# Performance work log

Hardware: AMD Instinct MI355X
Metric: run time of the kernel (lower is better)

## Reference

```python
import jax, jax.numpy as jnp
import numpy as np

GS = 8      # grid_size
NH = 8      # num_heads
DM = 256    # hidden_dim / d_model
B, W, H = 4, 256, 256


def setup_inputs() -> dict:
    key = jax.random.key(0)
    ks = jax.random.split(key, 5)
    s = 0.02
    return {
        "x": jax.random.normal(ks[0], (B, DM, W, H), dtype=jnp.float32),
        "Wq": jax.random.normal(ks[1], (DM, DM), dtype=jnp.float32) * s,
        "bq": jnp.zeros((DM,), dtype=jnp.float32),
        "Wk": jax.random.normal(ks[2], (DM, DM), dtype=jnp.float32) * s,
        "bk": jnp.zeros((DM,), dtype=jnp.float32),
        "Wv": jax.random.normal(ks[3], (DM, DM), dtype=jnp.float32) * s,
        "bv": jnp.zeros((DM,), dtype=jnp.float32),
        "Wo": jax.random.normal(ks[4], (DM, DM), dtype=jnp.float32) * s,
        "bo": jnp.zeros((DM,), dtype=jnp.float32),
    }


def reference(x, Wq, bq, Wk, bk, Wv, bv, Wo, bo):
    b, d, w, h = x.shape
    gw, gh = w // GS, h // GS
    n = gw * gh               # num grid cells
    L = GS * GS               # tokens per cell
    dh = d // NH

    # query: avg-pool each grid cell -> (b*n, 1, d)
    q = x.reshape(b, d, gw, GS, gh, GS).mean(axis=(3, 5))      # (b, d, gw, gh)
    q = q.reshape(b, d, n).transpose(0, 2, 1).reshape(b * n, 1, d)

    # K/V: per-cell patch tokens, (b*n, L, d); matches torch unfold layout
    kv = x.transpose(0, 2, 3, 1)                                # (b, w, h, d)
    kv = kv.reshape(b, gw, GS, gh, GS, d)
    kv = kv.transpose(0, 1, 3, 2, 4, 5).reshape(b * n, L, d)

    # multi-head cross-attention (standard: q/k/v/out linear + softmax)
    qp = (q @ Wq.T + bq).reshape(b * n, 1, NH, dh).transpose(0, 2, 1, 3)   # (bn, H, 1, dh)
    kp = (kv @ Wk.T + bk).reshape(b * n, L, NH, dh).transpose(0, 2, 1, 3)  # (bn, H, L, dh)
    vp = (kv @ Wv.T + bv).reshape(b * n, L, NH, dh).transpose(0, 2, 1, 3)

    scores = jnp.einsum("bhqd,bhkd->bhqk", qp, kp) / jnp.sqrt(jnp.float32(dh))
    attn = jax.nn.softmax(scores, axis=-1)                      # (bn, H, 1, L)
    ctx = jnp.einsum("bhqk,bhkd->bhqd", attn, vp)               # (bn, H, 1, dh)
    ctx = ctx.transpose(0, 2, 1, 3).reshape(b * n, 1, d)
    attn_out = ctx @ Wo.T + bo                                  # (bn, 1, d)

    out = q + attn_out
    return out.reshape(b, n, d)
```

## Files before the change

kernel.cpp:

```cpp
#include <hip/hip_runtime.h>
#include <hip/hip_bf16.h>


#define NCELL 4096

typedef float f32x4 __attribute__((ext_vector_type(4)));
typedef short s16x8 __attribute__((ext_vector_type(8)));

#define OFF_NT 0u
#define OFF_BE 262144u
#define OFF_Q 262400u
#define OFF_S 1310976u
#define OFF_WQB 5505280u
#define OFF_WKB 5538048u

__device__ __forceinline__ unsigned short bfrnd(float f) {
  unsigned u = __float_as_uint(f);
  u += 0x7fffu + ((u >> 16) & 1u);
  return (unsigned short)(u >> 16);
}
__device__ __forceinline__ float bflo(unsigned u) { return __uint_as_float(u << 16); }
__device__ __forceinline__ float bfhi(unsigned u) { return __uint_as_float(u & 0xffff0000u); }

__global__ __launch_bounds__(256) void k_cvt(const float* __restrict__ Wq, const float* __restrict__ Wk,
                                             unsigned short* __restrict__ WQB, unsigned short* __restrict__ WKB) {
  const int i = blockIdx.x * 256 + threadIdx.x;
  {
    const float4 v = *reinterpret_cast<const float4*>(Wq + i * 4);
    const unsigned lo = (unsigned)bfrnd(v.x) | ((unsigned)bfrnd(v.y) << 16);
    const unsigned hi = (unsigned)bfrnd(v.z) | ((unsigned)bfrnd(v.w) << 16);
    *reinterpret_cast<uint2*>(WQB + i * 4) = make_uint2(lo, hi);
  }
  {
    const float4 v = *reinterpret_cast<const float4*>(Wk + i * 4);
    const unsigned lo = (unsigned)bfrnd(v.x) | ((unsigned)bfrnd(v.y) << 16);
    const unsigned hi = (unsigned)bfrnd(v.z) | ((unsigned)bfrnd(v.w) << 16);
    *reinterpret_cast<uint2*>(WKB + i * 4) = make_uint2(lo, hi);
  }
}

__global__ __launch_bounds__(256) void k_nt(const float* __restrict__ Wv, const float* __restrict__ Wo,
                                            unsigned short* __restrict__ NT) {
  __shared__ float wo_s[32];
  const int n = blockIdx.x >> 3, h = blockIdx.x & 7;
  const int j = threadIdx.x;
  if (threadIdx.x < 32) wo_s[threadIdx.x] = Wo[n * 256 + h * 32 + threadIdx.x];
  __syncthreads();
  float acc = 0.f;
#pragma unroll
  for (int i = 0; i < 32; ++i) acc += Wv[(h * 32 + i) * 256 + j] * wo_s[i];
  NT[(size_t)n * 2048 + h * 256 + j] = bfrnd(acc);
}

__global__ __launch_bounds__(256) void k_beff(const float* __restrict__ bo, const float* __restrict__ bv,
                                              const float* __restrict__ Wo, float* __restrict__ BE) {
  const int w = threadIdx.x >> 6, l = threadIdx.x & 63;
  const int k = blockIdx.x * 4 + w;
  float acc = 0.f;
#pragma unroll
  for (int c = 0; c < 4; ++c) acc += bv[l + 64 * c] * Wo[k * 256 + l + 64 * c];
#pragma unroll
  for (int mk = 32; mk >= 1; mk >>= 1) acc += __shfl_xor(acc, mk);
  if (l == 0) BE[k] = acc + bo[k];
}

__global__ __launch_bounds__(256) void k_cell(
    const float* __restrict__ x,
    const unsigned short* __restrict__ WQB, const float* __restrict__ bq,
    const unsigned short* __restrict__ WKB, const float* __restrict__ bk,
    float* __restrict__ Qg, unsigned short* __restrict__ Sg) {
  __shared__ __align__(16) unsigned short xb[256 * 72];
  __shared__ __align__(16) float q_s[256];
  __shared__ __align__(16) float qp_s[256];
  __shared__ __align__(16) unsigned short r_bf[8 * 264];
  __shared__ __align__(16) float R1[2304];
  __shared__ float off_s[8];

  const int tid = threadIdx.x;
  const int cell = blockIdx.x;
  const int b = cell >> 10, cw = (cell >> 5) & 31, ch = cell & 31;
  const float* xp = x + (size_t)b * 16777216 + (size_t)cw * 2048 + (size_t)ch * 8;

#pragma unroll
  for (int it = 0; it < 16; ++it) {
    const int idx = it * 256 + tid;
    const int d = idx >> 4, i = (idx >> 1) & 7, half = idx & 1;
    const float4 v = *reinterpret_cast<const float4*>(xp + (size_t)d * 65536 + i * 256 + half * 4);
    const int t0 = i * 8 + half * 4;
    const unsigned lo = (unsigned)bfrnd(v.x) | ((unsigned)bfrnd(v.y) << 16);
    const unsigned hi = (unsigned)bfrnd(v.z) | ((unsigned)bfrnd(v.w) << 16);
    *reinterpret_cast<uint2*>(&xb[d * 72 + t0]) = make_uint2(lo, hi);
    float ps = (v.x + v.y) + (v.z + v.w);
    ps += __shfl_xor(ps, 1);
    ps += __shfl_xor(ps, 2);
    ps += __shfl_xor(ps, 4);
    ps += __shfl_xor(ps, 8);
    if ((tid & 15) == 0) {
      const float qv = ps * (1.0f / 64.0f);
      q_s[d] = qv;
      Qg[(size_t)cell * 256 + d] = qv;
    }
  }
  __syncthreads();

  {
    const int io = tid >> 5, jl = tid & 31;
    const float4 qa = *reinterpret_cast<const float4*>(&q_s[jl * 8]);
    const float4 qb = *reinterpret_cast<const float4*>(&q_s[jl * 8 + 4]);
#pragma unroll 4
    for (int r = 0; r < 32; ++r) {
      const int i = r * 8 + io;
      const uint4 wv = *reinterpret_cast<const uint4*>(WQB + i * 256 + jl * 8);
      float acc = bflo(wv.x) * qa.x + bfhi(wv.x) * qa.y + bflo(wv.y) * qa.z + bfhi(wv.y) * qa.w +
                  bflo(wv.z) * qb.x + bfhi(wv.z) * qb.y + bflo(wv.w) * qb.z + bfhi(wv.w) * qb.w;
      acc += __shfl_xor(acc, 16);
      acc += __shfl_xor(acc, 8);
      acc += __shfl_xor(acc, 4);
      acc += __shfl_xor(acc, 2);
      acc += __shfl_xor(acc, 1);
      if (jl == 0) qp_s[i] = (acc + bq[i]) * 0.17677669529663689f;
    }
  }
  __syncthreads();

  {
    const int hw = tid >> 6;
    const int j0 = (tid & 63) * 4;
#pragma unroll
    for (int hh = 0; hh < 2; ++hh) {
      const int h = hw * 2 + hh;
      float a0 = 0.f, a1 = 0.f, a2 = 0.f, a3 = 0.f;
#pragma unroll
      for (int i = 0; i < 32; ++i) {
        const float s = qp_s[h * 32 + i];
        const uint2 wv = *reinterpret_cast<const uint2*>(WKB + (h * 32 + i) * 256 + j0);
        a0 += s * bflo(wv.x);
        a1 += s * bfhi(wv.x);
        a2 += s * bflo(wv.y);
        a3 += s * bfhi(wv.y);
      }
      const unsigned lo = (unsigned)bfrnd(a0) | ((unsigned)bfrnd(a1) << 16);
      const unsigned hi = (unsigned)bfrnd(a2) | ((unsigned)bfrnd(a3) << 16);
      *reinterpret_cast<uint2*>(&r_bf[h * 264 + j0]) = make_uint2(lo, hi);
    }
    if (tid < 8) {
      float o = 0.f;
      for (int i = 0; i < 32; ++i) o += qp_s[tid * 32 + i] * bk[tid * 32 + i];
      off_s[tid] = o;
    }
  }
  __syncthreads();

  {
    const int t = tid & 63, p = tid >> 6;
    float xr[64];
#pragma unroll
    for (int dd = 0; dd < 64; ++dd) {
      const unsigned v = xb[(p * 64 + dd) * 72 + t];
      xr[dd] = __uint_as_float(v << 16);
    }
#pragma unroll
    for (int h = 0; h < 8; ++h) {
      float acc = 0.f;
#pragma unroll
      for (int dc = 0; dc < 8; ++dc) {
        const uint4 rv = *reinterpret_cast<const uint4*>(&r_bf[h * 264 + p * 64 + dc * 8]);
        acc += bflo(rv.x) * xr[dc * 8 + 0] + bfhi(rv.x) * xr[dc * 8 + 1] +
               bflo(rv.y) * xr[dc * 8 + 2] + bfhi(rv.y) * xr[dc * 8 + 3] +
               bflo(rv.z) * xr[dc * 8 + 4] + bfhi(rv.z) * xr[dc * 8 + 5] +
               bflo(rv.w) * xr[dc * 8 + 6] + bfhi(rv.w) * xr[dc * 8 + 7];
      }
      R1[p * 576 + t * 9 + h] = acc;
    }
  }
  __syncthreads();

  {
    const int w = tid >> 6, t = tid & 63;
    float av[2];
#pragma unroll
    for (int hi = 0; hi < 2; ++hi) {
      const int h = w + hi * 4;
      const float v = R1[0 * 576 + t * 9 + h] + R1[1 * 576 + t * 9 + h] +
                      R1[2 * 576 + t * 9 + h] + R1[3 * 576 + t * 9 + h] + off_s[h];
      float m = v;
#pragma unroll
      for (int mk = 32; mk >= 1; mk >>= 1) m = fmaxf(m, __shfl_xor(m, mk));
      const float e = __expf(v - m);
      float s = e;
#pragma unroll
      for (int mk = 32; mk >= 1; mk >>= 1) s += __shfl_xor(s, mk);
      av[hi] = e / s;
    }
    __syncthreads();
    R1[t * 12 + w] = av[0];
    R1[t * 12 + w + 4] = av[1];
  }
  __syncthreads();

  {
    const int d = tid;
    float acc[8] = {0, 0, 0, 0, 0, 0, 0, 0};
#pragma unroll
    for (int tc = 0; tc < 8; ++tc) {
      const uint4 xv = *reinterpret_cast<const uint4*>(&xb[d * 72 + tc * 8]);
      const float xf[8] = {bflo(xv.x), bfhi(xv.x), bflo(xv.y), bfhi(xv.y),
                           bflo(xv.z), bfhi(xv.z), bflo(xv.w), bfhi(xv.w)};
#pragma unroll
      for (int k = 0; k < 8; ++k) {
        const int t = tc * 8 + k;
        const float4 aA = *reinterpret_cast<const float4*>(&R1[t * 12]);
        const float4 aB = *reinterpret_cast<const float4*>(&R1[t * 12 + 4]);
        acc[0] += aA.x * xf[k]; acc[1] += aA.y * xf[k];
        acc[2] += aA.z * xf[k]; acc[3] += aA.w * xf[k];
        acc[4] += aB.x * xf[k]; acc[5] += aB.y * xf[k];
        acc[6] += aB.z * xf[k]; acc[7] += aB.w * xf[k];
      }
    }
#pragma unroll
    for (int h = 0; h < 8; ++h)
      Sg[(size_t)cell * 2048 + h * 256 + d] = bfrnd(acc[h]);
  }
}

__global__ __launch_bounds__(256) void k_out(
    const unsigned short* __restrict__ Sg, const unsigned short* __restrict__ NT,
    const float* __restrict__ Qg, const float* __restrict__ BE, float* __restrict__ out) {
  __shared__ __align__(16) unsigned short As[64 * 72];
  __shared__ __align__(16) unsigned short Bs[64 * 72];
  const int tid = threadIdx.x;
  const int m0 = (blockIdx.x >> 2) * 64, n0 = (blockIdx.x & 3) * 64;
  const int w = tid >> 6, l = tid & 63;
  const int wm = (w & 1) * 32, wn = (w >> 1) * 32;
  const int lr = l & 15, lq = l >> 4;

  f32x4 acc[2][2];
#pragma unroll
  for (int a = 0; a < 2; ++a)
#pragma unroll
    for (int c = 0; c < 2; ++c) acc[a][c] = (f32x4){0.f, 0.f, 0.f, 0.f};

  const int srow = tid >> 2, sseg = tid & 3;
  for (int kt = 0; kt < 32; ++kt) {
    const int k0 = kt * 64;
    const uint4 a0v = *reinterpret_cast<const uint4*>(&Sg[(size_t)(m0 + srow) * 2048 + k0 + sseg * 16]);
    const uint4 a1v = *reinterpret_cast<const uint4*>(&Sg[(size_t)(m0 + srow) * 2048 + k0 + sseg * 16 + 8]);
    const uint4 b0v = *reinterpret_cast<const uint4*>(&NT[(size_t)(n0 + srow) * 2048 + k0 + sseg * 16]);
    const uint4 b1v = *reinterpret_cast<const uint4*>(&NT[(size_t)(n0 + srow) * 2048 + k0 + sseg * 16 + 8]);
    __syncthreads();
    *reinterpret_cast<uint4*>(&As[srow * 72 + sseg * 16]) = a0v;
    *reinterpret_cast<uint4*>(&As[srow * 72 + sseg * 16 + 8]) = a1v;
    *reinterpret_cast<uint4*>(&Bs[srow * 72 + sseg * 16]) = b0v;
    *reinterpret_cast<uint4*>(&Bs[srow * 72 + sseg * 16 + 8]) = b1v;
    __syncthreads();
#pragma unroll
    for (int s = 0; s < 2; ++s) {
      s16x8 af[2], bfr[2];
#pragma unroll
      for (int a = 0; a < 2; ++a)
        af[a] = *reinterpret_cast<const s16x8*>(&As[(wm + a * 16 + lr) * 72 + s * 32 + lq * 8]);
#pragma unroll
      for (int c = 0; c < 2; ++c)
        bfr[c] = *reinterpret_cast<const s16x8*>(&Bs[(wn + c * 16 + lr) * 72 + s * 32 + lq * 8]);
#pragma unroll
      for (int a = 0; a < 2; ++a)
#pragma unroll
        for (int c = 0; c < 2; ++c)
          acc[a][c] = __builtin_amdgcn_mfma_f32_16x16x32_bf16(af[a], bfr[c], acc[a][c], 0, 0, 0);
    }
  }
#pragma unroll
  for (int a = 0; a < 2; ++a) {
#pragma unroll
    for (int c = 0; c < 2; ++c) {
      const int col = n0 + wn + c * 16 + lr;
#pragma unroll
      for (int rr = 0; rr < 4; ++rr) {
        const int row = m0 + wm + a * 16 + lq * 4 + rr;
        out[(size_t)row * 256 + col] = acc[a][c][rr] + Qg[(size_t)row * 256 + col] + BE[col];
      }
    }
  }
}

extern "C" void kernel_launch(void* const* d_in, const int* in_sizes, int n_in,
                              void* d_out, int out_size, void* d_ws, size_t ws_size,
                              hipStream_t stream) {
  const float* x = (const float*)d_in[0];
  const float* Wq = (const float*)d_in[1];
  const float* bq = (const float*)d_in[2];
  const float* Wk = (const float*)d_in[3];
  const float* bk = (const float*)d_in[4];
  const float* Wv = (const float*)d_in[5];
  const float* bv = (const float*)d_in[6];
  const float* Wo = (const float*)d_in[7];
  const float* bo = (const float*)d_in[8];
  float* ws = (float*)d_ws;
  unsigned short* NT = (unsigned short*)(ws + OFF_NT);
  float* BE = ws + OFF_BE;
  float* Qg = ws + OFF_Q;
  unsigned short* Sg = (unsigned short*)(ws + OFF_S);
  unsigned short* WQB = (unsigned short*)(ws + OFF_WQB);
  unsigned short* WKB = (unsigned short*)(ws + OFF_WKB);
  float* out = (float*)d_out;

  hipLaunchKernelGGL(k_cvt, dim3(64), dim3(256), 0, stream, Wq, Wk, WQB, WKB);
  hipLaunchKernelGGL(k_nt, dim3(2048), dim3(256), 0, stream, Wv, Wo, NT);
  hipLaunchKernelGGL(k_beff, dim3(64), dim3(256), 0, stream, bo, bv, Wo, BE);
  hipLaunchKernelGGL(k_cell, dim3(NCELL), dim3(256), 0, stream, x, WQB, bq, WKB, bk, Qg, Sg);
  hipLaunchKernelGGL(k_out, dim3(256), dim3(256), 0, stream, Sg, NT, Qg, BE, out);
}
```

Baseline: 676.8 us.

## Split-K the output GEMM with atomics, fuse residual into cell kernel, batch loads

The output GEMM is split four ways along K (1024 blocks instead of 256) and its partial results are accumulated into the output with atomicAdd. The cell kernel writes q+bias straight into the output, so the Qg buffer goes away. The cell kernel also issues all 16 x loads up front, remaps block indices to spread cells across batches, and batches four Wq dot products so their shuffle reductions interleave. The GEMM register-prefetches the next K tile, and both kernels get launch-bounds occupancy hints. Atomic accumulation adds contention and makes the float summation order nondeterministic.

Result: no change. 687.9 us (+1.6%).

```diff
diff --git a/kernel.cpp b/kernel.cpp
--- a/kernel.cpp
+++ b/kernel.cpp
@@ -9,7 +9,6 @@
 
 #define OFF_NT 0u
 #define OFF_BE 262144u
-#define OFF_Q 262400u
 #define OFF_S 1310976u
 #define OFF_WQB 5505280u
 #define OFF_WKB 5538048u
@@ -64,11 +63,12 @@
   if (l == 0) BE[k] = acc + bo[k];
 }
 
-__global__ __launch_bounds__(256) void k_cell(
+__global__ __launch_bounds__(256, 3) void k_cell(
     const float* __restrict__ x,
     const unsigned short* __restrict__ WQB, const float* __restrict__ bq,
     const unsigned short* __restrict__ WKB, const float* __restrict__ bk,
-    float* __restrict__ Qg, unsigned short* __restrict__ Sg) {
+    const float* __restrict__ BE,
+    float* __restrict__ out, unsigned short* __restrict__ Sg) {
   __shared__ __align__(16) unsigned short xb[256 * 72];
   __shared__ __align__(16) float q_s[256];
   __shared__ __align__(16) float qp_s[256];
@@ -77,48 +77,61 @@
   __shared__ float off_s[8];
 
   const int tid = threadIdx.x;
-  const int cell = blockIdx.x;
+  const int cell = ((blockIdx.x & 7) << 9) | (blockIdx.x >> 3);
   const int b = cell >> 10, cw = (cell >> 5) & 31, ch = cell & 31;
   const float* xp = x + (size_t)b * 16777216 + (size_t)cw * 2048 + (size_t)ch * 8;
 
+  const int i_row = (tid >> 1) & 7, half = tid & 1, d0 = tid >> 4;
+  const float* tb = xp + (size_t)d0 * 65536 + i_row * 256 + half * 4;
+  float4 v[16];
+#pragma unroll
+  for (int it = 0; it < 16; ++it)
+    v[it] = *reinterpret_cast<const float4*>(tb + (size_t)it * 1048576);
+  const int t0 = i_row * 8 + half * 4;
 #pragma unroll
   for (int it = 0; it < 16; ++it) {
-    const int idx = it * 256 + tid;
-    const int d = idx >> 4, i = (idx >> 1) & 7, half = idx & 1;
-    const float4 v = *reinterpret_cast<const float4*>(xp + (size_t)d * 65536 + i * 256 + half * 4);
-    const int t0 = i * 8 + half * 4;
-    const unsigned lo = (unsigned)bfrnd(v.x) | ((unsigned)bfrnd(v.y) << 16);
-    const unsigned hi = (unsigned)bfrnd(v.z) | ((unsigned)bfrnd(v.w) << 16);
+    const int d = it * 16 + d0;
+    const unsigned lo = (unsigned)bfrnd(v[it].x) | ((unsigned)bfrnd(v[it].y) << 16);
+    const unsigned hi = (unsigned)bfrnd(v[it].z) | ((unsigned)bfrnd(v[it].w) << 16);
     *reinterpret_cast<uint2*>(&xb[d * 72 + t0]) = make_uint2(lo, hi);
-    float ps = (v.x + v.y) + (v.z + v.w);
+    float ps = (v[it].x + v[it].y) + (v[it].z + v[it].w);
     ps += __shfl_xor(ps, 1);
     ps += __shfl_xor(ps, 2);
     ps += __shfl_xor(ps, 4);
     ps += __shfl_xor(ps, 8);
-    if ((tid & 15) == 0) {
-      const float qv = ps * (1.0f / 64.0f);
-      q_s[d] = qv;
-      Qg[(size_t)cell * 256 + d] = qv;
-    }
-  }
-  __syncthreads();
+    if ((tid & 15) == 0) q_s[d] = ps * (1.0f / 64.0f);
+  }
+  __syncthreads();
+
+  out[(size_t)cell * 256 + tid] = q_s[tid] + BE[tid];
 
   {
     const int io = tid >> 5, jl = tid & 31;
-    const float4 qa = *reinterpret_cast<const float4*>(&q_s[jl * 8]);
-    const float4 qb = *reinterpret_cast<const float4*>(&q_s[jl * 8 + 4]);
-#pragma unroll 4
-    for (int r = 0; r < 32; ++r) {
-      const int i = r * 8 + io;
-      const uint4 wv = *reinterpret_cast<const uint4*>(WQB + i * 256 + jl * 8);
-      float acc = bflo(wv.x) * qa.x + bfhi(wv.x) * qa.y + bflo(wv.y) * qa.z + bfhi(wv.y) * qa.w +
-                  bflo(wv.z) * qb.x + bfhi(wv.z) * qb.y + bflo(wv.w) * qb.z + bfhi(wv.w) * qb.w;
-      acc += __shfl_xor(acc, 16);
-      acc += __shfl_xor(acc, 8);
-      acc += __shfl_xor(acc, 4);
-      acc += __shfl_xor(acc, 2);
-      acc += __shfl_xor(acc, 1);
-      if (jl == 0) qp_s[i] = (acc + bq[i]) * 0.17677669529663689f;
+    float qr[8];
+    *reinterpret_cast<float4*>(qr) = *reinterpret_cast<const float4*>(&q_s[jl * 8]);
+    *reinterpret_cast<float4*>(qr + 4) = *reinterpret_cast<const float4*>(&q_s[jl * 8 + 4]);
+#pragma unroll
+    for (int rb = 0; rb < 8; ++rb) {
+      float acc[4];
+#pragma unroll
+      for (int rr = 0; rr < 4; ++rr) {
+        const int i = (rb * 4 + rr) * 8 + io;
+        const uint4 wv = *reinterpret_cast<const uint4*>(WQB + i * 256 + jl * 8);
+        acc[rr] = bflo(wv.x) * qr[0] + bfhi(wv.x) * qr[1] + bflo(wv.y) * qr[2] + bfhi(wv.y) * qr[3] +
+                  bflo(wv.z) * qr[4] + bfhi(wv.z) * qr[5] + bflo(wv.w) * qr[6] + bfhi(wv.w) * qr[7];
+      }
+#pragma unroll
+      for (int mk = 16; mk >= 1; mk >>= 1) {
+#pragma unroll
+        for (int rr = 0; rr < 4; ++rr) acc[rr] += __shfl_xor(acc[rr], mk);
+      }
+      if (jl == 0) {
+#pragma unroll
+        for (int rr = 0; rr < 4; ++rr) {
+          const int i = (rb * 4 + rr) * 8 + io;
+          qp_s[i] = (acc[rr] + bq[i]) * 0.17677669529663689f;
+        }
+      }
     }
   }
   __syncthreads();
@@ -156,8 +169,8 @@
     float xr[64];
 #pragma unroll
     for (int dd = 0; dd < 64; ++dd) {
-      const unsigned v = xb[(p * 64 + dd) * 72 + t];
-      xr[dd] = __uint_as_float(v << 16);
+      const unsigned vv = xb[(p * 64 + dd) * 72 + t];
+      xr[dd] = __uint_as_float(vv << 16);
     }
 #pragma unroll
     for (int h = 0; h < 8; ++h) {
@@ -181,12 +194,12 @@
 #pragma unroll
     for (int hi = 0; hi < 2; ++hi) {
       const int h = w + hi * 4;
-      const float v = R1[0 * 576 + t * 9 + h] + R1[1 * 576 + t * 9 + h] +
-                      R1[2 * 576 + t * 9 + h] + R1[3 * 576 + t * 9 + h] + off_s[h];
-      float m = v;
+      const float vv = R1[0 * 576 + t * 9 + h] + R1[1 * 576 + t * 9 + h] +
+                       R1[2 * 576 + t * 9 + h] + R1[3 * 576 + t * 9 + h] + off_s[h];
+      float m = vv;
 #pragma unroll
       for (int mk = 32; mk >= 1; mk >>= 1) m = fmaxf(m, __shfl_xor(m, mk));
-      const float e = __expf(v - m);
+      const float e = __expf(vv - m);
       float s = e;
 #pragma unroll
       for (int mk = 32; mk >= 1; mk >>= 1) s += __shfl_xor(s, mk);
@@ -223,13 +236,14 @@
   }
 }
 
-__global__ __launch_bounds__(256) void k_out(
+__global__ __launch_bounds__(256, 4) void k_out(
     const unsigned short* __restrict__ Sg, const unsigned short* __restrict__ NT,
-    const float* __restrict__ Qg, const float* __restrict__ BE, float* __restrict__ out) {
+    float* __restrict__ out) {
   __shared__ __align__(16) unsigned short As[64 * 72];
   __shared__ __align__(16) unsigned short Bs[64 * 72];
   const int tid = threadIdx.x;
-  const int m0 = (blockIdx.x >> 2) * 64, n0 = (blockIdx.x & 3) * 64;
+  const int tile = blockIdx.x >> 2, ks = blockIdx.x & 3;
+  const int m0 = (tile >> 2) * 64, n0 = (tile & 3) * 64;
   const int w = tid >> 6, l = tid & 63;
   const int wm = (w & 1) * 32, wn = (w >> 1) * 32;
   const int lr = l & 15, lq = l >> 4;
@@ -241,18 +255,29 @@
     for (int c = 0; c < 2; ++c) acc[a][c] = (f32x4){0.f, 0.f, 0.f, 0.f};
 
   const int srow = tid >> 2, sseg = tid & 3;
-  for (int kt = 0; kt < 32; ++kt) {
-    const int k0 = kt * 64;
-    const uint4 a0v = *reinterpret_cast<const uint4*>(&Sg[(size_t)(m0 + srow) * 2048 + k0 + sseg * 16]);
-    const uint4 a1v = *reinterpret_cast<const uint4*>(&Sg[(size_t)(m0 + srow) * 2048 + k0 + sseg * 16 + 8]);
-    const uint4 b0v = *reinterpret_cast<const uint4*>(&NT[(size_t)(n0 + srow) * 2048 + k0 + sseg * 16]);
-    const uint4 b1v = *reinterpret_cast<const uint4*>(&NT[(size_t)(n0 + srow) * 2048 + k0 + sseg * 16 + 8]);
+  const size_t arow = (size_t)(m0 + srow) * 2048 + sseg * 16;
+  const size_t brow = (size_t)(n0 + srow) * 2048 + sseg * 16;
+  const int kbase = ks * 512;
+
+  uint4 a0v = *reinterpret_cast<const uint4*>(&Sg[arow + kbase]);
+  uint4 a1v = *reinterpret_cast<const uint4*>(&Sg[arow + kbase + 8]);
+  uint4 b0v = *reinterpret_cast<const uint4*>(&NT[brow + kbase]);
+  uint4 b1v = *reinterpret_cast<const uint4*>(&NT[brow + kbase + 8]);
+
+  for (int kt = 0; kt < 8; ++kt) {
     __syncthreads();
     *reinterpret_cast<uint4*>(&As[srow * 72 + sseg * 16]) = a0v;
     *reinterpret_cast<uint4*>(&As[srow * 72 + sseg * 16 + 8]) = a1v;
     *reinterpret_cast<uint4*>(&Bs[srow * 72 + sseg * 16]) = b0v;
     *reinterpret_cast<uint4*>(&Bs[srow * 72 + sseg * 16 + 8]) = b1v;
     __syncthreads();
+    if (kt < 7) {
+      const int kn = kbase + (kt + 1) * 64;
+      a0v = *reinterpret_cast<const uint4*>(&Sg[arow + kn]);
+      a1v = *reinterpret_cast<const uint4*>(&Sg[arow + kn + 8]);
+      b0v = *reinterpret_cast<const uint4*>(&NT[brow + kn]);
+      b1v = *reinterpret_cast<const uint4*>(&NT[brow + kn + 8]);
+    }
 #pragma unroll
     for (int s = 0; s < 2; ++s) {
       s16x8 af[2], bfr[2];
@@ -277,7 +302,7 @@
 #pragma unroll
       for (int rr = 0; rr < 4; ++rr) {
         const int row = m0 + wm + a * 16 + lq * 4 + rr;
-        out[(size_t)row * 256 + col] = acc[a][c][rr] + Qg[(size_t)row * 256 + col] + BE[col];
+        atomicAdd(&out[(size_t)row * 256 + col], acc[a][c][rr]);
       }
     }
   }
@@ -298,7 +323,6 @@
   float* ws = (float*)d_ws;
   unsigned short* NT = (unsigned short*)(ws + OFF_NT);
   float* BE = ws + OFF_BE;
-  float* Qg = ws + OFF_Q;
   unsigned short* Sg = (unsigned short*)(ws + OFF_S);
   unsigned short* WQB = (unsigned short*)(ws + OFF_WQB);
   unsigned short* WKB = (unsigned short*)(ws + OFF_WKB);
@@ -307,6 +331,6 @@
   hipLaunchKernelGGL(k_cvt, dim3(64), dim3(256), 0, stream, Wq, Wk, WQB, WKB);
   hipLaunchKernelGGL(k_nt, dim3(2048), dim3(256), 0, stream, Wv, Wo, NT);
   hipLaunchKernelGGL(k_beff, dim3(64), dim3(256), 0, stream, bo, bv, Wo, BE);
-  hipLaunchKernelGGL(k_cell, dim3(NCELL), dim3(256), 0, stream, x, WQB, bq, WKB, bk, Qg, Sg);
-  hipLaunchKernelGGL(k_out, dim3(256), dim3(256), 0, stream, Sg, NT, Qg, BE, out);
-}
+  hipLaunchKernelGGL(k_cell, dim3(NCELL), dim3(256), 0, stream, x, WQB, bq, WKB, bk, BE, out, Sg);
+  hipLaunchKernelGGL(k_out, dim3(1024), dim3(256), 0, stream, Sg, NT, out);
+}
```
